# Kernel tuning notes

Hardware: AMD Instinct MI355X
Metric: run time of the kernel (lower is better)

Reference implementation:

```python
import jax, jax.numpy as jnp
import numpy as np

HEADS = 8
HID = 256
EPS = 1e-5  # fp32 path of the custom LayerNorm


def setup_inputs() -> dict:
    key = jax.random.key(0)
    k1, k2, k3, k4 = jax.random.split(key, 4)
    B, C, H, W = 16, 256, 64, 64
    x = jax.random.normal(k1, (B, C, H, W), dtype=jnp.float32)
    # Conv2d 1x1 weights as matrices [out_ch, in_ch]
    w_qkv = jax.random.normal(k2, (3 * HID, C), dtype=jnp.float32) * (1.0 / np.sqrt(C))
    w_out = jax.random.normal(k3, (C, HID), dtype=jnp.float32) * (1.0 / np.sqrt(HID))
    b_out = jax.random.normal(k4, (C,), dtype=jnp.float32) * 0.01
    g = jnp.ones((C,), dtype=jnp.float32)
    return {"x": x, "w_qkv": w_qkv, "w_out": w_out, "b_out": b_out, "g": g}


def reference(x, w_qkv, w_out, b_out, g):
    B, C, H, W = x.shape
    n = H * W
    dh = HID // HEADS
    scale = dh ** -0.5

    # 1x1 conv == per-pixel GEMM: [B,3*HID,H,W]
    qkv = jnp.einsum('bchw,oc->bohw', x, w_qkv)
    qkv = qkv.reshape(B, 3, HEADS, dh, n)          # b 3 h d n
    q, k, v = qkv[:, 0], qkv[:, 1], qkv[:, 2]      # each [B,h,d,n]

    q = jax.nn.softmax(q, axis=2) * scale          # softmax over head-dim d
    k = jax.nn.softmax(k, axis=3)                  # softmax over spatial n
    v = v / n

    context = jnp.einsum('bhdn,bhen->bhde', k, v)  # [B,h,d,d] tiny per-head context
    out = jnp.einsum('bhde,bhdn->bhen', context, q)  # [B,h,d,n]
    out = out.reshape(B, HID, H, W)

    y = jnp.einsum('bchw,oc->bohw', out, w_out) + b_out[None, :, None, None]

    # channel LayerNorm (biased var), per original module
    mean = jnp.mean(y, axis=1, keepdims=True)
    var = jnp.var(y, axis=1, keepdims=True)
    return (y - mean) * jax.lax.rsqrt(var + EPS) * g[None, :, None, None]
```

## Files before the change

### kernel.cpp

```cpp
#include <hip/hip_runtime.h>
#include <hip/hip_bf16.h>
#include <math.h>


typedef __attribute__((ext_vector_type(8))) short bf16x8;
typedef __attribute__((ext_vector_type(4))) float f32x4;
typedef __attribute__((ext_vector_type(8))) unsigned short u16x8;

#define GL16(g, l) __builtin_amdgcn_global_load_lds( \
    (__attribute__((address_space(1))) void*)(void*)(g), \
    (__attribute__((address_space(3))) void*)(void*)(l), 16, 0, 0)

__device__ inline float b2f(unsigned short u) {
    union { float f; unsigned int i; } v; v.i = ((unsigned int)u) << 16; return v.f;
}
__device__ inline unsigned short f2b(float f) {
    union { float f; unsigned int i; } v; v.f = f;
    unsigned int r = v.i + 0x7fff + ((v.i >> 16) & 1);
    return (unsigned short)(r >> 16);
}

__global__ __launch_bounds__(256) void conv_w(
    const float* __restrict__ wq, const float* __restrict__ wo,
    unsigned short* __restrict__ dst)
{
    int i4 = (blockIdx.x * 256 + threadIdx.x) * 4;
    float4 v = (i4 < 196608) ? *(const float4*)&wq[i4]
                             : *(const float4*)&wo[i4 - 196608];
    unsigned int lo = (unsigned int)f2b(v.x) | ((unsigned int)f2b(v.y) << 16);
    unsigned int hi = (unsigned int)f2b(v.z) | ((unsigned int)f2b(v.w) << 16);
    *(uint2*)&dst[i4] = make_uint2(lo, hi);
}

__global__ __launch_bounds__(256) void conv_x(
    const float* __restrict__ x, unsigned short* __restrict__ xt)
{
    __shared__ __align__(16) unsigned short T[64][72];
    const int t = threadIdx.x;
    const int p0 = blockIdx.x * 64, c0 = blockIdx.y * 64, b = blockIdx.z;
    const float* xb = x + ((size_t)b * 256 + c0) * 4096 + p0;
    #pragma unroll
    for (int i = 0; i < 4; ++i) {
        int flat = i * 256 + t;
        int cl = flat >> 4, p4 = (flat & 15) * 4;
        float4 v = *(const float4*)&xb[(size_t)cl * 4096 + p4];
        T[p4 + 0][cl] = f2b(v.x);
        T[p4 + 1][cl] = f2b(v.y);
        T[p4 + 2][cl] = f2b(v.z);
        T[p4 + 3][cl] = f2b(v.w);
    }
    __syncthreads();
    unsigned short* xtb = xt + ((size_t)b * 4096 + p0) * 256 + c0;
    #pragma unroll
    for (int j = 0; j < 2; ++j) {
        int flat = j * 256 + t;
        int row = flat >> 3, ch = flat & 7;
        uint4 v = *(const uint4*)&T[row][ch * 8];
        *(uint4*)&xtb[(size_t)row * 256 + ch * 8] = v;
    }
}

__global__ __launch_bounds__(256) void qkv_mfma(
    const unsigned short* __restrict__ wq,
    const unsigned short* __restrict__ xt,
    unsigned short* __restrict__ qkv)
{
    __shared__ __align__(16) unsigned short As[128 * 64];
    __shared__ __align__(16) unsigned short Bs[128 * 64];
    const int t = threadIdx.x;
    const int l = t & 63, w = t >> 6;
    const int lm = l & 15, kg = l >> 4, le = l & 7, l3 = l >> 3;
    const int sx8 = (le ^ l3) * 8;
    const int p0 = blockIdx.x * 128, o0 = blockIdx.y * 128, b = blockIdx.z;
    const int wo = (w >> 1) * 64, wp = (w & 1) * 64;

    f32x4 acc[4][4] = {};
    const unsigned short* xb = xt + (size_t)b * 4096 * 256;

    for (int ks = 0; ks < 4; ++ks) {
        const int e0 = ks * 64;
        #pragma unroll
        for (int i = 0; i < 4; ++i) {
            int cid = w * 4 + i;
            int m = cid * 8 + l3;
            GL16(wq + (size_t)(o0 + m) * 256 + e0 + sx8, &As[cid * 512]);
            GL16(xb + (size_t)(p0 + m) * 256 + e0 + sx8, &Bs[cid * 512]);
        }
        __syncthreads();
        #pragma unroll
        for (int s = 0; s < 2; ++s) {
            bf16x8 af[4], bfr[4];
            #pragma unroll
            for (int mi = 0; mi < 4; ++mi) {
                int row = wo + mi * 16 + lm;
                int ch = ((s * 4 + kg) ^ (row & 7)) * 8;
                af[mi] = *(const bf16x8*)&As[row * 64 + ch];
            }
            #pragma unroll
            for (int ni = 0; ni < 4; ++ni) {
                int row = wp + ni * 16 + lm;
                int ch = ((s * 4 + kg) ^ (row & 7)) * 8;
                bfr[ni] = *(const bf16x8*)&Bs[row * 64 + ch];
            }
            #pragma unroll
            for (int mi = 0; mi < 4; ++mi)
                #pragma unroll
                for (int ni = 0; ni < 4; ++ni)
                    acc[mi][ni] = __builtin_amdgcn_mfma_f32_16x16x32_bf16(
                        af[mi], bfr[ni], acc[mi][ni], 0, 0, 0);
        }
        __syncthreads();
    }
    unsigned short* ob = qkv + (size_t)b * 768 * 4096;
    #pragma unroll
    for (int mi = 0; mi < 4; ++mi)
        #pragma unroll
        for (int ni = 0; ni < 4; ++ni) {
            int o = o0 + wo + mi * 16 + kg * 4;
            int p = p0 + wp + ni * 16 + lm;
            #pragma unroll
            for (int r = 0; r < 4; ++r)
                ob[(size_t)(o + r) * 4096 + p] = f2b(acc[mi][ni][r]);
        }
}

__global__ __launch_bounds__(256) void kstats(
    const unsigned short* __restrict__ qkv,
    float* __restrict__ kmax, float* __restrict__ krecip)
{
    const int row = blockIdx.x;
    const int b = row >> 8, cd = row & 255;
    const int t = threadIdx.x;
    const unsigned short* kp = qkv + ((size_t)b * 768 + 256 + cd) * 4096 + t * 16;
    float v[16]; float m = -1e30f;
    u16x8 a0 = *(const u16x8*)kp;
    u16x8 a1 = *(const u16x8*)(kp + 8);
    #pragma unroll
    for (int i = 0; i < 8; ++i) { v[i] = b2f(a0[i]); v[8 + i] = b2f(a1[i]); }
    #pragma unroll
    for (int i = 0; i < 16; ++i) m = fmaxf(m, v[i]);
    #pragma unroll
    for (int off = 32; off > 0; off >>= 1) m = fmaxf(m, __shfl_xor(m, off));
    __shared__ float red[8];
    if ((t & 63) == 0) red[t >> 6] = m;
    __syncthreads();
    m = fmaxf(fmaxf(red[0], red[1]), fmaxf(red[2], red[3]));
    float s = 0.f;
    #pragma unroll
    for (int i = 0; i < 16; ++i) s += __expf(v[i] - m);
    #pragma unroll
    for (int off = 32; off > 0; off >>= 1) s += __shfl_xor(s, off);
    __syncthreads();
    if ((t & 63) == 0) red[4 + (t >> 6)] = s;
    __syncthreads();
    if (t == 0) {
        float S = red[4] + red[5] + red[6] + red[7];
        kmax[row] = m;
        krecip[row] = 1.0f / (S * 4096.0f);
    }
}

__global__ __launch_bounds__(256) void ctx_partial(
    const unsigned short* __restrict__ qkv,
    const float* __restrict__ kmax, const float* __restrict__ krecip,
    float* __restrict__ part)
{
    const int seg = blockIdx.x, bh = blockIdx.y;
    const int b = bh >> 3, h = bh & 7;
    const int t = threadIdx.x;
    __shared__ float kc[32][65];
    __shared__ __align__(16) float vt[64][36];
    const unsigned short* kb = qkv + ((size_t)b * 768 + 256 + h * 32) * 4096;
    const unsigned short* vb = qkv + ((size_t)b * 768 + 512 + h * 32) * 4096;
    const int d = t >> 3, e0 = (t & 7) * 4;
    float a0 = 0, a1 = 0, a2 = 0, a3 = 0;

    for (int ch = 0; ch < 8; ++ch) {
        const int pb = seg * 512 + ch * 64;
        #pragma unroll
        for (int r = 0; r < 4; ++r) {
            int dd = r * 8 + (t >> 5);
            int pp = (t & 31) * 2;
            unsigned int kraw = *(const unsigned int*)&kb[(size_t)dd * 4096 + pb + pp];
            float mx = kmax[bh * 32 + dd], rc = krecip[bh * 32 + dd];
            kc[dd][pp]     = __expf(b2f((unsigned short)(kraw & 0xffff)) - mx) * rc;
            kc[dd][pp + 1] = __expf(b2f((unsigned short)(kraw >> 16)) - mx) * rc;
            unsigned int vraw = *(const unsigned int*)&vb[(size_t)dd * 4096 + pb + pp];
            vt[pp][dd]     = b2f((unsigned short)(vraw & 0xffff));
            vt[pp + 1][dd] = b2f((unsigned short)(vraw >> 16));
        }
        __syncthreads();
        #pragma unroll
        for (int pp = 0; pp < 64; ++pp) {
            float kd = kc[d][pp];
            float4 v4 = *(const float4*)&vt[pp][e0];
            a0 += kd * v4.x; a1 += kd * v4.y; a2 += kd * v4.z; a3 += kd * v4.w;
        }
        __syncthreads();
    }
    float* pp = part + ((size_t)(bh * 8 + seg) * 32 + d) * 32 + e0;
    pp[0] = a0; pp[1] = a1; pp[2] = a2; pp[3] = a3;
}

__global__ __launch_bounds__(256) void ctx_reduce(
    const float* __restrict__ part, float* __restrict__ ctxt)
{
    const int bh = blockIdx.x; const int t = threadIdx.x;
    #pragma unroll
    for (int r = 0; r < 4; ++r) {
        int idx = r * 256 + t;
        int d = idx >> 5, e = idx & 31;
        float s = 0.f;
        #pragma unroll
        for (int sg = 0; sg < 8; ++sg) s += part[((size_t)bh * 8 + sg) * 1024 + idx];
        ctxt[(size_t)bh * 1024 + e * 32 + d] = s;
    }
}

__global__ __launch_bounds__(256) void qctx(
    const unsigned short* __restrict__ qkv,
    const float* __restrict__ ctxt,
    unsigned short* __restrict__ outt)
{
    __shared__ __align__(16) float ctx_s[8192];
    __shared__ unsigned short out_s[64][258];
    const int t = threadIdx.x;
    const int pb = blockIdx.x * 64, b = blockIdx.y;
    {
        const float4* src = (const float4*)(ctxt + (size_t)b * 8192);
        float4* dst = (float4*)ctx_s;
        #pragma unroll
        for (int i = 0; i < 8; ++i) dst[i * 256 + t] = src[i * 256 + t];
    }
    __syncthreads();
    const int w = t >> 6, p = t & 63;
    const float scale = 0.17677669529663689f;
    #pragma unroll
    for (int hh = 0; hh < 2; ++hh) {
        const int h = w * 2 + hh;
        const unsigned short* qb = qkv + ((size_t)b * 768 + h * 32) * 4096 + pb + p;
        float ex[32]; float m = -1e30f;
        #pragma unroll
        for (int d = 0; d < 32; ++d) { ex[d] = b2f(qb[(size_t)d * 4096]); m = fmaxf(m, ex[d]); }
        float s = 0.f;
        #pragma unroll
        for (int d = 0; d < 32; ++d) { ex[d] = __expf(ex[d] - m); s += ex[d]; }
        const float inv = scale / s;
        const float* cb = ctx_s + h * 1024;
        #pragma unroll
        for (int e = 0; e < 32; ++e) {
            const float4* cr = (const float4*)(cb + e * 32);
            float a = 0.f;
            #pragma unroll
            for (int d4 = 0; d4 < 8; ++d4) {
                float4 c4 = cr[d4];
                a += c4.x * ex[d4 * 4] + c4.y * ex[d4 * 4 + 1]
                   + c4.z * ex[d4 * 4 + 2] + c4.w * ex[d4 * 4 + 3];
            }
            out_s[p][h * 32 + e] = f2b(a * inv);
        }
    }
    __syncthreads();
    unsigned int* ob = (unsigned int*)outt;
    #pragma unroll
    for (int j = 0; j < 32; ++j) {
        int flat = j * 256 + t;
        int row = flat >> 7, cw = flat & 127;
        unsigned int v = *(const unsigned int*)&out_s[row][cw * 2];
        ob[(size_t)(b * 4096 + pb + row) * 128 + cw] = v;
    }
}

__global__ __launch_bounds__(256) void proj_ln(
    const unsigned short* __restrict__ woutb,
    const unsigned short* __restrict__ outt,
    const float* __restrict__ b_out, const float* __restrict__ g,
    float* __restrict__ y)
{
    __shared__ __align__(16) unsigned short As[256 * 64];
    __shared__ __align__(16) unsigned short Bs[64 * 64];
    __shared__ float red1[4][64], red2[4][64], mean_s[64], rstd_s[64];
    const int t = threadIdx.x;
    const int l = t & 63, w = t >> 6;
    const int lm = l & 15, kg = l >> 4, le = l & 7, l3 = l >> 3;
    const int sx8 = (le ^ l3) * 8;
    const int pb = blockIdx.x * 64, b = blockIdx.y;

    f32x4 acc[4][4] = {};
    const unsigned short* outb = outt + (size_t)b * 4096 * 256;

    for (int ks = 0; ks < 4; ++ks) {
        const int e0 = ks * 64;
        #pragma unroll
        for (int i = 0; i < 8; ++i) {
            int cid = w * 8 + i;
            int m = cid * 8 + l3;
            GL16(woutb + (size_t)m * 256 + e0 + sx8, &As[cid * 512]);
        }
        #pragma unroll
        for (int i = 0; i < 2; ++i) {
            int cid = w * 2 + i;
            int m = cid * 8 + l3;
            GL16(outb + (size_t)(pb + m) * 256 + e0 + sx8, &Bs[cid * 512]);
        }
        __syncthreads();
        #pragma unroll
        for (int s = 0; s < 2; ++s) {
            bf16x8 af[4], bfr[4];
            #pragma unroll
            for (int mi = 0; mi < 4; ++mi) {
                int row = w * 64 + mi * 16 + lm;
                int ch = ((s * 4 + kg) ^ (row & 7)) * 8;
                af[mi] = *(const bf16x8*)&As[row * 64 + ch];
            }
            #pragma unroll
            for (int ni = 0; ni < 4; ++ni) {
                int row = ni * 16 + lm;
                int ch = ((s * 4 + kg) ^ (row & 7)) * 8;
                bfr[ni] = *(const bf16x8*)&Bs[row * 64 + ch];
            }
            #pragma unroll
            for (int mi = 0; mi < 4; ++mi)
                #pragma unroll
                for (int ni = 0; ni < 4; ++ni)
                    acc[mi][ni] = __builtin_amdgcn_mfma_f32_16x16x32_bf16(
                        af[mi], bfr[ni], acc[mi][ni], 0, 0, 0);
        }
        __syncthreads();
    }
    float bo[4][4], gv[4][4];
    #pragma unroll
    for (int mi = 0; mi < 4; ++mi)
        #pragma unroll
        for (int r = 0; r < 4; ++r) {
            int c = w * 64 + mi * 16 + kg * 4 + r;
            bo[mi][r] = b_out[c]; gv[mi][r] = g[c];
        }
    #pragma unroll
    for (int mi = 0; mi < 4; ++mi)
        #pragma unroll
        for (int ni = 0; ni < 4; ++ni)
            #pragma unroll
            for (int r = 0; r < 4; ++r)
                acc[mi][ni][r] += bo[mi][r];
    #pragma unroll
    for (int ni = 0; ni < 4; ++ni) {
        float s1 = 0.f, s2 = 0.f;
        #pragma unroll
        for (int mi = 0; mi < 4; ++mi)
            #pragma unroll
            for (int r = 0; r < 4; ++r) { float v = acc[mi][ni][r]; s1 += v; s2 += v * v; }
        s1 += __shfl_xor(s1, 16); s2 += __shfl_xor(s2, 16);
        s1 += __shfl_xor(s1, 32); s2 += __shfl_xor(s2, 32);
        if (kg == 0) { red1[w][ni * 16 + lm] = s1; red2[w][ni * 16 + lm] = s2; }
    }
    __syncthreads();
    if (t < 64) {
        float s1 = red1[0][t] + red1[1][t] + red1[2][t] + red1[3][t];
        float s2 = red2[0][t] + red2[1][t] + red2[2][t] + red2[3][t];
        float mn = s1 * (1.f / 256.f);
        float var = s2 * (1.f / 256.f) - mn * mn;
        mean_s[t] = mn; rstd_s[t] = rsqrtf(var + 1e-5f);
    }
    __syncthreads();
    float* yb = y + (size_t)b * 256 * 4096 + pb;
    #pragma unroll
    for (int ni = 0; ni < 4; ++ni) {
        int p = ni * 16 + lm;
        float mn = mean_s[p], rs = rstd_s[p];
        #pragma unroll
        for (int mi = 0; mi < 4; ++mi) {
            int c = w * 64 + mi * 16 + kg * 4;
            #pragma unroll
            for (int r = 0; r < 4; ++r)
                yb[(size_t)(c + r) * 4096 + p] = (acc[mi][ni][r] - mn) * rs * gv[mi][r];
        }
    }
}

extern "C" void kernel_launch(void* const* d_in, const int* in_sizes, int n_in,
                              void* d_out, int out_size, void* d_ws, size_t ws_size,
                              hipStream_t stream) {
    const float* x     = (const float*)d_in[0];
    const float* w_qkv = (const float*)d_in[1];
    const float* w_out = (const float*)d_in[2];
    const float* b_out = (const float*)d_in[3];
    const float* g     = (const float*)d_in[4];
    float* y = (float*)d_out;

    char* ws = (char*)d_ws;
    unsigned short* qkvb  = (unsigned short*)ws;
    unsigned short* xt    = (unsigned short*)(ws + 100663296);
    unsigned short* wbf   = (unsigned short*)(ws + 134217728);
    float*          kmax  = (float*)(ws + 134742016);
    float*          krec  = (float*)(ws + 134758400);
    float*          part  = (float*)(ws + 134774784);
    float*          ctxt  = (float*)(ws + 138969088);
    unsigned short* outt  = (unsigned short*)(ws + 139493376);

    conv_w<<<256, 256, 0, stream>>>(w_qkv, w_out, wbf);
    conv_x<<<dim3(64, 4, 16), 256, 0, stream>>>(x, xt);
    qkv_mfma<<<dim3(32, 6, 16), 256, 0, stream>>>(wbf, xt, qkvb);
    kstats<<<4096, 256, 0, stream>>>(qkvb, kmax, krec);
    ctx_partial<<<dim3(8, 128), 256, 0, stream>>>(qkvb, kmax, krec, part);
    ctx_reduce<<<128, 256, 0, stream>>>(part, ctxt);
    qctx<<<dim3(64, 16), 256, 0, stream>>>(qkvb, ctxt, outt);
    proj_ln<<<dim3(64, 16), 256, 0, stream>>>(wbf + 196608, outt, b_out, g, y);
}
```

Before: 272.0 us.

## Fuse q-context product and output projection with LayerNorm into one MFMA kernel

Merges the qctx and proj_ln kernels into a single attn_out kernel. The q softmax, the context multiply (now done with bf16 MFMA against a bf16 context written by ctx_reduce) and the output projection plus channel LayerNorm all run per 64-pixel tile while the intermediate stays in shared memory. This removes the global write and re-read of the 32MB intermediate outt and one kernel launch. In exchange, the context is rounded to bf16, the w_out chunks are reloaded per block with extra barriers, and the epilogue goes through a staged shared-memory transpose.

```diff
diff --git a/kernel.cpp b/kernel.cpp
--- a/kernel.cpp
+++ b/kernel.cpp
@@ -203,177 +203,150 @@
 }
 
 __global__ __launch_bounds__(256) void ctx_reduce(
-    const float* __restrict__ part, float* __restrict__ ctxt)
+    const float* __restrict__ part, unsigned short* __restrict__ ctxb)
 {
     const int bh = blockIdx.x; const int t = threadIdx.x;
     #pragma unroll
     for (int r = 0; r < 4; ++r) {
-        int idx = r * 256 + t;
-        int d = idx >> 5, e = idx & 31;
+        int oi = r * 256 + t;
+        int e = oi >> 5, d = oi & 31;
         float s = 0.f;
         #pragma unroll
-        for (int sg = 0; sg < 8; ++sg) s += part[((size_t)bh * 8 + sg) * 1024 + idx];
-        ctxt[(size_t)bh * 1024 + e * 32 + d] = s;
-    }
-}
-
-__global__ __launch_bounds__(256) void qctx(
+        for (int sg = 0; sg < 8; ++sg) s += part[((size_t)bh * 8 + sg) * 1024 + d * 32 + e];
+        ctxb[(size_t)bh * 1024 + oi] = f2b(s);
+    }
+}
+
+#define RS 260
+__global__ __launch_bounds__(256) void attn_out(
     const unsigned short* __restrict__ qkv,
-    const float* __restrict__ ctxt,
-    unsigned short* __restrict__ outt)
-{
-    __shared__ __align__(16) float ctx_s[8192];
-    __shared__ unsigned short out_s[64][258];
-    const int t = threadIdx.x;
-    const int pb = blockIdx.x * 64, b = blockIdx.y;
-    {
-        const float4* src = (const float4*)(ctxt + (size_t)b * 8192);
-        float4* dst = (float4*)ctx_s;
-        #pragma unroll
-        for (int i = 0; i < 8; ++i) dst[i * 256 + t] = src[i * 256 + t];
-    }
-    __syncthreads();
-    const int w = t >> 6, p = t & 63;
-    const float scale = 0.17677669529663689f;
-    #pragma unroll
-    for (int hh = 0; hh < 2; ++hh) {
-        const int h = w * 2 + hh;
-        const unsigned short* qb = qkv + ((size_t)b * 768 + h * 32) * 4096 + pb + p;
-        float ex[32]; float m = -1e30f;
-        #pragma unroll
-        for (int d = 0; d < 32; ++d) { ex[d] = b2f(qb[(size_t)d * 4096]); m = fmaxf(m, ex[d]); }
-        float s = 0.f;
-        #pragma unroll
-        for (int d = 0; d < 32; ++d) { ex[d] = __expf(ex[d] - m); s += ex[d]; }
-        const float inv = scale / s;
-        const float* cb = ctx_s + h * 1024;
-        #pragma unroll
-        for (int e = 0; e < 32; ++e) {
-            const float4* cr = (const float4*)(cb + e * 32);
-            float a = 0.f;
-            #pragma unroll
-            for (int d4 = 0; d4 < 8; ++d4) {
-                float4 c4 = cr[d4];
-                a += c4.x * ex[d4 * 4] + c4.y * ex[d4 * 4 + 1]
-                   + c4.z * ex[d4 * 4 + 2] + c4.w * ex[d4 * 4 + 3];
-            }
-            out_s[p][h * 32 + e] = f2b(a * inv);
-        }
-    }
-    __syncthreads();
-    unsigned int* ob = (unsigned int*)outt;
-    #pragma unroll
-    for (int j = 0; j < 32; ++j) {
-        int flat = j * 256 + t;
-        int row = flat >> 7, cw = flat & 127;
-        unsigned int v = *(const unsigned int*)&out_s[row][cw * 2];
-        ob[(size_t)(b * 4096 + pb + row) * 128 + cw] = v;
-    }
-}
-
-__global__ __launch_bounds__(256) void proj_ln(
+    const unsigned short* __restrict__ ctxb,
     const unsigned short* __restrict__ woutb,
-    const unsigned short* __restrict__ outt,
     const float* __restrict__ b_out, const float* __restrict__ g,
     float* __restrict__ y)
 {
-    __shared__ __align__(16) unsigned short As[256 * 64];
-    __shared__ __align__(16) unsigned short Bs[64 * 64];
-    __shared__ float red1[4][64], red2[4][64], mean_s[64], rstd_s[64];
-    const int t = threadIdx.x;
-    const int l = t & 63, w = t >> 6;
-    const int lm = l & 15, kg = l >> 4, le = l & 7, l3 = l >> 3;
-    const int sx8 = (le ^ l3) * 8;
-    const int pb = blockIdx.x * 64, b = blockIdx.y;
-
-    f32x4 acc[4][4] = {};
-    const unsigned short* outb = outt + (size_t)b * 4096 * 256;
-
-    for (int ks = 0; ks < 4; ++ks) {
-        const int e0 = ks * 64;
-        #pragma unroll
-        for (int i = 0; i < 8; ++i) {
-            int cid = w * 8 + i;
-            int m = cid * 8 + l3;
-            GL16(woutb + (size_t)m * 256 + e0 + sx8, &As[cid * 512]);
-        }
-        #pragma unroll
-        for (int i = 0; i < 2; ++i) {
-            int cid = w * 2 + i;
-            int m = cid * 8 + l3;
-            GL16(outb + (size_t)(pb + m) * 256 + e0 + sx8, &Bs[cid * 512]);
-        }
-        __syncthreads();
-        #pragma unroll
-        for (int s = 0; s < 2; ++s) {
-            bf16x8 af[4], bfr[4];
-            #pragma unroll
-            for (int mi = 0; mi < 4; ++mi) {
-                int row = w * 64 + mi * 16 + lm;
-                int ch = ((s * 4 + kg) ^ (row & 7)) * 8;
-                af[mi] = *(const bf16x8*)&As[row * 64 + ch];
+    __shared__ __align__(16) unsigned char smem[34816];
+    unsigned short* qT  = (unsigned short*)smem;
+    unsigned short* wch = (unsigned short*)smem;
+    float*          fb  = (float*)smem;
+
+    const int t = threadIdx.x, l = t & 63, w = t >> 6;
+    const int lm = l & 15, kg = l >> 4;
+    const int p0 = blockIdx.x * 64, b = blockIdx.y;
+    const int wp = w * 16;
+
+    const unsigned short* qb = qkv + (size_t)b * 768 * 4096 + p0;
+    #pragma unroll
+    for (int i = 0; i < 8; ++i) {
+        int flat = i * 256 + t;
+        int o = flat >> 3, j = flat & 7;
+        u16x8 v = *(const u16x8*)&qb[(size_t)o * 4096 + j * 8];
+        #pragma unroll
+        for (int s = 0; s < 8; ++s) qT[(j * 8 + s) * RS + o] = (unsigned short)v[s];
+    }
+    __syncthreads();
+
+    const float scale = 0.17677669529663689f;
+    #pragma unroll
+    for (int h = 0; h < 8; ++h) {
+        bf16x8 araw = *(const bf16x8*)&qT[(wp + lm) * RS + h * 32 + kg * 8];
+        float ex[8]; float m = -1e30f;
+        #pragma unroll
+        for (int i = 0; i < 8; ++i) { ex[i] = b2f((unsigned short)araw[i]); m = fmaxf(m, ex[i]); }
+        m = fmaxf(m, __shfl_xor(m, 16)); m = fmaxf(m, __shfl_xor(m, 32));
+        float s = 0.f;
+        #pragma unroll
+        for (int i = 0; i < 8; ++i) { ex[i] = __expf(ex[i] - m); s += ex[i]; }
+        s += __shfl_xor(s, 16); s += __shfl_xor(s, 32);
+        const float inv = scale / s;
+        bf16x8 a1;
+        #pragma unroll
+        for (int i = 0; i < 8; ++i) a1[i] = (short)f2b(ex[i] * inv);
+        const unsigned short* cb = ctxb + ((size_t)(b * 8 + h)) * 1024;
+        bf16x8 b1a = *(const bf16x8*)&cb[lm * 32 + kg * 8];
+        bf16x8 b1b = *(const bf16x8*)&cb[(16 + lm) * 32 + kg * 8];
+        f32x4 c0 = {0.f, 0.f, 0.f, 0.f}, c1 = {0.f, 0.f, 0.f, 0.f};
+        c0 = __builtin_amdgcn_mfma_f32_16x16x32_bf16(a1, b1a, c0, 0, 0, 0);
+        c1 = __builtin_amdgcn_mfma_f32_16x16x32_bf16(a1, b1b, c1, 0, 0, 0);
+        #pragma unroll
+        for (int r = 0; r < 4; ++r) {
+            int p = wp + kg * 4 + r;
+            qT[p * RS + h * 32 + lm]      = f2b(c0[r]);
+            qT[p * RS + h * 32 + 16 + lm] = f2b(c1[r]);
+        }
+    }
+    bf16x8 a2[8];
+    #pragma unroll
+    for (int kc = 0; kc < 8; ++kc)
+        a2[kc] = *(const bf16x8*)&qT[(wp + lm) * RS + kc * 32 + kg * 8];
+
+    f32x4 c2[16];
+    #pragma unroll
+    for (int ct = 0; ct < 16; ++ct) c2[ct] = (f32x4){0.f, 0.f, 0.f, 0.f};
+    for (int kc = 0; kc < 8; ++kc) {
+        __syncthreads();
+        #pragma unroll
+        for (int i = 0; i < 4; ++i) {
+            int flat = i * 256 + t;
+            int c = flat >> 2, j = flat & 3;
+            u16x8 v = *(const u16x8*)&woutb[(size_t)c * 256 + kc * 32 + j * 8];
+            *(u16x8*)&wch[c * 36 + j * 8] = v;
+        }
+        __syncthreads();
+        #pragma unroll
+        for (int ct = 0; ct < 16; ++ct) {
+            bf16x8 b2 = *(const bf16x8*)&wch[(ct * 16 + lm) * 36 + kg * 8];
+            c2[ct] = __builtin_amdgcn_mfma_f32_16x16x32_bf16(a2[kc], b2, c2[ct], 0, 0, 0);
+        }
+    }
+
+    float bias[16], gam[16];
+    #pragma unroll
+    for (int ct = 0; ct < 16; ++ct) { bias[ct] = b_out[ct * 16 + lm]; gam[ct] = g[ct * 16 + lm]; }
+    float s1[4] = {0.f, 0.f, 0.f, 0.f}, s2[4] = {0.f, 0.f, 0.f, 0.f};
+    #pragma unroll
+    for (int ct = 0; ct < 16; ++ct)
+        #pragma unroll
+        for (int r = 0; r < 4; ++r) {
+            float v = c2[ct][r] + bias[ct];
+            c2[ct][r] = v; s1[r] += v; s2[r] += v * v;
+        }
+    #pragma unroll
+    for (int off = 1; off < 16; off <<= 1) {
+        #pragma unroll
+        for (int r = 0; r < 4; ++r) { s1[r] += __shfl_xor(s1[r], off); s2[r] += __shfl_xor(s2[r], off); }
+    }
+    float mn[4], rsd[4];
+    #pragma unroll
+    for (int r = 0; r < 4; ++r) {
+        mn[r] = s1[r] * (1.f / 256.f);
+        float var = s2[r] * (1.f / 256.f) - mn[r] * mn[r];
+        rsd[r] = rsqrtf(var + 1e-5f);
+    }
+
+    float* ybase = y + (size_t)b * 256 * 4096 + p0;
+    for (int pass = 0; pass < 2; ++pass) {
+        __syncthreads();
+        #pragma unroll
+        for (int ct8 = 0; ct8 < 8; ++ct8) {
+            int ct = pass * 8 + ct8;
+            int row = ct8 * 16 + lm;
+            int chunk = (wp >> 2) + kg;
+            int chs = (chunk ^ (row & 7)) * 4;
+            #pragma unroll
+            for (int r = 0; r < 4; ++r)
+                fb[row * 68 + chs + r] = (c2[ct][r] - mn[r]) * rsd[r] * gam[ct];
+        }
+        __syncthreads();
+        {
+            int row = t >> 1, half = t & 1;
+            int cg = pass * 128 + row;
+            #pragma unroll
+            for (int j = 0; j < 8; ++j) {
+                int chunk = (half * 8 + j) ^ (row & 7);
+                float4 v = *(const float4*)&fb[row * 68 + chunk * 4];
+                *(float4*)&ybase[(size_t)cg * 4096 + half * 32 + j * 4] = v;
             }
-            #pragma unroll
-            for (int ni = 0; ni < 4; ++ni) {
-                int row = ni * 16 + lm;
-                int ch = ((s * 4 + kg) ^ (row & 7)) * 8;
-                bfr[ni] = *(const bf16x8*)&Bs[row * 64 + ch];
-            }
-            #pragma unroll
-            for (int mi = 0; mi < 4; ++mi)
-                #pragma unroll
-                for (int ni = 0; ni < 4; ++ni)
-                    acc[mi][ni] = __builtin_amdgcn_mfma_f32_16x16x32_bf16(
-                        af[mi], bfr[ni], acc[mi][ni], 0, 0, 0);
-        }
-        __syncthreads();
-    }
-    float bo[4][4], gv[4][4];
-    #pragma unroll
-    for (int mi = 0; mi < 4; ++mi)
-        #pragma unroll
-        for (int r = 0; r < 4; ++r) {
-            int c = w * 64 + mi * 16 + kg * 4 + r;
-            bo[mi][r] = b_out[c]; gv[mi][r] = g[c];
-        }
-    #pragma unroll
-    for (int mi = 0; mi < 4; ++mi)
-        #pragma unroll
-        for (int ni = 0; ni < 4; ++ni)
-            #pragma unroll
-            for (int r = 0; r < 4; ++r)
-                acc[mi][ni][r] += bo[mi][r];
-    #pragma unroll
-    for (int ni = 0; ni < 4; ++ni) {
-        float s1 = 0.f, s2 = 0.f;
-        #pragma unroll
-        for (int mi = 0; mi < 4; ++mi)
-            #pragma unroll
-            for (int r = 0; r < 4; ++r) { float v = acc[mi][ni][r]; s1 += v; s2 += v * v; }
-        s1 += __shfl_xor(s1, 16); s2 += __shfl_xor(s2, 16);
-        s1 += __shfl_xor(s1, 32); s2 += __shfl_xor(s2, 32);
-        if (kg == 0) { red1[w][ni * 16 + lm] = s1; red2[w][ni * 16 + lm] = s2; }
-    }
-    __syncthreads();
-    if (t < 64) {
-        float s1 = red1[0][t] + red1[1][t] + red1[2][t] + red1[3][t];
-        float s2 = red2[0][t] + red2[1][t] + red2[2][t] + red2[3][t];
-        float mn = s1 * (1.f / 256.f);
-        float var = s2 * (1.f / 256.f) - mn * mn;
-        mean_s[t] = mn; rstd_s[t] = rsqrtf(var + 1e-5f);
-    }
-    __syncthreads();
-    float* yb = y + (size_t)b * 256 * 4096 + pb;
-    #pragma unroll
-    for (int ni = 0; ni < 4; ++ni) {
-        int p = ni * 16 + lm;
-        float mn = mean_s[p], rs = rstd_s[p];
-        #pragma unroll
-        for (int mi = 0; mi < 4; ++mi) {
-            int c = w * 64 + mi * 16 + kg * 4;
-            #pragma unroll
-            for (int r = 0; r < 4; ++r)
-                yb[(size_t)(c + r) * 4096 + p] = (acc[mi][ni][r] - mn) * rs * gv[mi][r];
         }
     }
 }
@@ -395,15 +368,13 @@
     float*          kmax  = (float*)(ws + 134742016);
     float*          krec  = (float*)(ws + 134758400);
     float*          part  = (float*)(ws + 134774784);
-    float*          ctxt  = (float*)(ws + 138969088);
-    unsigned short* outt  = (unsigned short*)(ws + 139493376);
+    unsigned short* ctxb  = (unsigned short*)(ws + 138969088);
 
     conv_w<<<256, 256, 0, stream>>>(w_qkv, w_out, wbf);
     conv_x<<<dim3(64, 4, 16), 256, 0, stream>>>(x, xt);
     qkv_mfma<<<dim3(32, 6, 16), 256, 0, stream>>>(wbf, xt, qkvb);
     kstats<<<4096, 256, 0, stream>>>(qkvb, kmax, krec);
     ctx_partial<<<dim3(8, 128), 256, 0, stream>>>(qkvb, kmax, krec, part);
-    ctx_reduce<<<128, 256, 0, stream>>>(part, ctxt);
-    qctx<<<dim3(64, 16), 256, 0, stream>>>(qkvb, ctxt, outt);
-    proj_ln<<<dim3(64, 16), 256, 0, stream>>>(wbf + 196608, outt, b_out, g, y);
-}
+    ctx_reduce<<<128, 256, 0, stream>>>(part, ctxb);
+    attn_out<<<dim3(64, 16), 256, 0, stream>>>(qkvb, ctxb, wbf + 196608, b_out, g, y);
+}
```

Measured after the change: 393.4 us. +44.6%, slower.

## Compute q·context with bf16 MFMA and store context in bf16

Applied to the files above, without the earlier changes.

Rewrites the q-context stage so each wavefront computes the per-head softmax over the head dimension, split across lanes with shuffle reductions. It then applies the 32x32 context through two 16x16x32 bf16 MFMA instructions instead of scalar fp32 FMAs out of LDS. ctx_reduce now writes the context transposed to bf16, which shrinks the load and removes the LDS staging of the fp32 context. Softmax weights and context are rounded to bf16 before the matmul, which adds some precision loss.

```diff
diff --git a/kernel.cpp b/kernel.cpp
--- a/kernel.cpp
+++ b/kernel.cpp
@@ -203,71 +203,70 @@
 }
 
 __global__ __launch_bounds__(256) void ctx_reduce(
-    const float* __restrict__ part, float* __restrict__ ctxt)
+    const float* __restrict__ part, unsigned short* __restrict__ ctxb)
 {
     const int bh = blockIdx.x; const int t = threadIdx.x;
     #pragma unroll
     for (int r = 0; r < 4; ++r) {
-        int idx = r * 256 + t;
-        int d = idx >> 5, e = idx & 31;
+        int oi = r * 256 + t;
+        int e = oi >> 5, d = oi & 31;
         float s = 0.f;
         #pragma unroll
-        for (int sg = 0; sg < 8; ++sg) s += part[((size_t)bh * 8 + sg) * 1024 + idx];
-        ctxt[(size_t)bh * 1024 + e * 32 + d] = s;
-    }
-}
-
-__global__ __launch_bounds__(256) void qctx(
+        for (int sg = 0; sg < 8; ++sg) s += part[((size_t)bh * 8 + sg) * 1024 + d * 32 + e];
+        ctxb[(size_t)bh * 1024 + oi] = f2b(s);
+    }
+}
+
+#define RS 260
+__global__ __launch_bounds__(256) void qctx2(
     const unsigned short* __restrict__ qkv,
-    const float* __restrict__ ctxt,
+    const unsigned short* __restrict__ ctxb,
     unsigned short* __restrict__ outt)
 {
-    __shared__ __align__(16) float ctx_s[8192];
-    __shared__ unsigned short out_s[64][258];
-    const int t = threadIdx.x;
-    const int pb = blockIdx.x * 64, b = blockIdx.y;
-    {
-        const float4* src = (const float4*)(ctxt + (size_t)b * 8192);
-        float4* dst = (float4*)ctx_s;
-        #pragma unroll
-        for (int i = 0; i < 8; ++i) dst[i * 256 + t] = src[i * 256 + t];
-    }
-    __syncthreads();
-    const int w = t >> 6, p = t & 63;
+    __shared__ unsigned short outw[4][16][RS];
+    const int t = threadIdx.x, l = t & 63, w = t >> 6;
+    const int lm = l & 15, kg = l >> 4;
+    const int p0 = blockIdx.x * 64, b = blockIdx.y;
+    const int wp = w * 16;
     const float scale = 0.17677669529663689f;
-    #pragma unroll
-    for (int hh = 0; hh < 2; ++hh) {
-        const int h = w * 2 + hh;
-        const unsigned short* qb = qkv + ((size_t)b * 768 + h * 32) * 4096 + pb + p;
-        float ex[32]; float m = -1e30f;
-        #pragma unroll
-        for (int d = 0; d < 32; ++d) { ex[d] = b2f(qb[(size_t)d * 4096]); m = fmaxf(m, ex[d]); }
+
+    const unsigned short* qb = qkv + (size_t)b * 768 * 4096 + p0 + wp + lm;
+    #pragma unroll
+    for (int h = 0; h < 8; ++h) {
+        float ex[8]; float m = -1e30f;
+        #pragma unroll
+        for (int i = 0; i < 8; ++i) {
+            ex[i] = b2f(qb[(size_t)(h * 32 + kg * 8 + i) * 4096]);
+            m = fmaxf(m, ex[i]);
+        }
+        m = fmaxf(m, __shfl_xor(m, 16)); m = fmaxf(m, __shfl_xor(m, 32));
         float s = 0.f;
         #pragma unroll
-        for (int d = 0; d < 32; ++d) { ex[d] = __expf(ex[d] - m); s += ex[d]; }
+        for (int i = 0; i < 8; ++i) { ex[i] = __expf(ex[i] - m); s += ex[i]; }
+        s += __shfl_xor(s, 16); s += __shfl_xor(s, 32);
         const float inv = scale / s;
-        const float* cb = ctx_s + h * 1024;
-        #pragma unroll
-        for (int e = 0; e < 32; ++e) {
-            const float4* cr = (const float4*)(cb + e * 32);
-            float a = 0.f;
-            #pragma unroll
-            for (int d4 = 0; d4 < 8; ++d4) {
-                float4 c4 = cr[d4];
-                a += c4.x * ex[d4 * 4] + c4.y * ex[d4 * 4 + 1]
-                   + c4.z * ex[d4 * 4 + 2] + c4.w * ex[d4 * 4 + 3];
-            }
-            out_s[p][h * 32 + e] = f2b(a * inv);
-        }
-    }
-    __syncthreads();
-    unsigned int* ob = (unsigned int*)outt;
-    #pragma unroll
-    for (int j = 0; j < 32; ++j) {
-        int flat = j * 256 + t;
-        int row = flat >> 7, cw = flat & 127;
-        unsigned int v = *(const unsigned int*)&out_s[row][cw * 2];
-        ob[(size_t)(b * 4096 + pb + row) * 128 + cw] = v;
+        bf16x8 a1;
+        #pragma unroll
+        for (int i = 0; i < 8; ++i) a1[i] = (short)f2b(ex[i] * inv);
+        const unsigned short* cb = ctxb + ((size_t)(b * 8 + h)) * 1024;
+        bf16x8 b1a = *(const bf16x8*)&cb[lm * 32 + kg * 8];
+        bf16x8 b1b = *(const bf16x8*)&cb[(16 + lm) * 32 + kg * 8];
+        f32x4 c0 = {0.f, 0.f, 0.f, 0.f}, c1 = {0.f, 0.f, 0.f, 0.f};
+        c0 = __builtin_amdgcn_mfma_f32_16x16x32_bf16(a1, b1a, c0, 0, 0, 0);
+        c1 = __builtin_amdgcn_mfma_f32_16x16x32_bf16(a1, b1b, c1, 0, 0, 0);
+        #pragma unroll
+        for (int r = 0; r < 4; ++r) {
+            outw[w][kg * 4 + r][h * 32 + lm]      = f2b(c0[r]);
+            outw[w][kg * 4 + r][h * 32 + 16 + lm] = f2b(c1[r]);
+        }
+    }
+
+    unsigned short* ob = outt + ((size_t)(b * 4096 + p0 + wp)) * 256;
+    #pragma unroll
+    for (int pass = 0; pass < 8; ++pass) {
+        int row = l >> 2, ec = (l & 3) * 8 + pass * 32;
+        u16x8 v = *(const u16x8*)&outw[w][row][ec];
+        *(u16x8*)&ob[(size_t)row * 256 + ec] = v;
     }
 }
 
@@ -395,15 +394,15 @@
     float*          kmax  = (float*)(ws + 134742016);
     float*          krec  = (float*)(ws + 134758400);
     float*          part  = (float*)(ws + 134774784);
-    float*          ctxt  = (float*)(ws + 138969088);
-    unsigned short* outt  = (unsigned short*)(ws + 139493376);
+    unsigned short* ctxb  = (unsigned short*)(ws + 138969088);
+    unsigned short* outt  = (unsigned short*)(ws + 139231232);
 
     conv_w<<<256, 256, 0, stream>>>(w_qkv, w_out, wbf);
     conv_x<<<dim3(64, 4, 16), 256, 0, stream>>>(x, xt);
     qkv_mfma<<<dim3(32, 6, 16), 256, 0, stream>>>(wbf, xt, qkvb);
     kstats<<<4096, 256, 0, stream>>>(qkvb, kmax, krec);
     ctx_partial<<<dim3(8, 128), 256, 0, stream>>>(qkvb, kmax, krec, part);
-    ctx_reduce<<<128, 256, 0, stream>>>(part, ctxt);
-    qctx<<<dim3(64, 16), 256, 0, stream>>>(qkvb, ctxt, outt);
+    ctx_reduce<<<128, 256, 0, stream>>>(part, ctxb);
+    qctx2<<<dim3(64, 16), 256, 0, stream>>>(qkvb, ctxb, outt);
     proj_ln<<<dim3(64, 16), 256, 0, stream>>>(wbf + 196608, outt, b_out, g, y);
 }
```

Result: faster. 255.2 us (-6.2%).
